# Kernel tuning notes

Hardware: AMD Instinct MI355X
Metric: run time of the kernel (lower is better)

Reference implementation:

```python
import jax, jax.numpy as jnp
import numpy as np

N = 50000      # nodes
E = 400000     # edges
IN_DIM = 128
HID = 64
HEADS1 = 4
OUT_DIM = 64
NEG_SLOPE = 0.2


def _gat_layer(x, W, attn_l, attn_r, bias, src, dst, heads, out_feats):
    # x: [N, F_in]; W: [F_in, heads*out]; attn_l/attn_r: [heads, out]; bias: [heads*out]
    n = x.shape[0]
    feat = (x @ W).reshape(n, heads, out_feats)              # [N, H, D]
    el = jnp.sum(feat * attn_l, axis=-1)                     # [N, H]
    er = jnp.sum(feat * attn_r, axis=-1)                     # [N, H]
    e = jax.nn.leaky_relu(el[src] + er[dst], NEG_SLOPE)      # [E, H]
    # segment softmax over incoming edges per destination node
    emax = jax.ops.segment_max(e, dst, num_segments=n)       # [N, H]
    ex = jnp.exp(e - emax[dst])                              # [E, H]
    denom = jax.ops.segment_sum(ex, dst, num_segments=n)     # [N, H]
    alpha = ex / denom[dst]                                  # [E, H]
    msg = alpha[:, :, None] * feat[src]                      # [E, H, D]
    rst = jax.ops.segment_sum(msg, dst, num_segments=n)      # [N, H, D]
    return rst + bias.reshape(1, heads, out_feats)


def setup_inputs() -> dict:
    key = jax.random.key(0)
    ks = jax.random.split(key, 12)
    features = jax.random.normal(ks[0], (N, IN_DIM), dtype=jnp.float32)
    src = jax.random.randint(ks[1], (E,), 0, N, dtype=jnp.int32)
    dst = jax.random.randint(ks[2], (E,), 0, N, dtype=jnp.int32)
    s1 = 1.0 / np.sqrt(IN_DIM)
    s2 = 1.0 / np.sqrt(HEADS1 * HID)
    W1 = jax.random.normal(ks[3], (IN_DIM, HEADS1 * HID), dtype=jnp.float32) * s1
    attn_l1 = jax.random.normal(ks[4], (HEADS1, HID), dtype=jnp.float32) * 0.1
    attn_r1 = jax.random.normal(ks[5], (HEADS1, HID), dtype=jnp.float32) * 0.1
    b1 = jnp.zeros((HEADS1 * HID,), dtype=jnp.float32)
    W2 = jax.random.normal(ks[6], (HEADS1 * HID, OUT_DIM), dtype=jnp.float32) * s2
    attn_l2 = jax.random.normal(ks[7], (1, OUT_DIM), dtype=jnp.float32) * 0.1
    attn_r2 = jax.random.normal(ks[8], (1, OUT_DIM), dtype=jnp.float32) * 0.1
    b2 = jnp.zeros((OUT_DIM,), dtype=jnp.float32)
    return {"features": features, "src": src, "dst": dst,
            "W1": W1, "attn_l1": attn_l1, "attn_r1": attn_r1, "b1": b1,
            "W2": W2, "attn_l2": attn_l2, "attn_r2": attn_r2, "b2": b2}


def reference(features, src, dst, W1, attn_l1, attn_r1, b1, W2, attn_l2, attn_r2, b2):
    h = _gat_layer(features, W1, attn_l1, attn_r1, b1, src, dst, HEADS1, HID)  # [N, 4, 64]
    h = h.reshape(h.shape[0], -1)                                             # flatten heads
    h = _gat_layer(h, W2, attn_l2, attn_r2, b2, src, dst, 1, OUT_DIM)         # [N, 1, 64]
    return h
```

## Files before the change

kernel.cpp:

```cpp
#include <hip/hip_runtime.h>
#include <hip/hip_bf16.h>

#define N_NODES 50000
#define N_EDGES 400000
#define IN_DIM 128
#define HID 64
#define HEADS 4
#define L1_OUT (HEADS * HID)
#define OUT_DIM 64
#define NEG_SLOPE 0.2f
#define SCAN_B 256
#define HIST_B 1563

typedef short bf16x8 __attribute__((ext_vector_type(8)));
typedef float f32x4 __attribute__((ext_vector_type(4)));

__device__ __forceinline__ float leaky(float x) { return x > 0.f ? x : NEG_SLOPE * x; }

__device__ __forceinline__ unsigned short bfh(float x) {
    unsigned u = __float_as_uint(x);
    return (unsigned short)((u + 0x7fffu + ((u >> 16) & 1u)) >> 16);
}
__device__ __forceinline__ float fb(unsigned short h) {
    return __uint_as_float(((unsigned)h) << 16);
}

__global__ void hist_wprep_kernel(const int* __restrict__ dst, int* __restrict__ cnt,
                                  const float* __restrict__ W1, const float* __restrict__ W2,
                                  unsigned short* __restrict__ W1fh, unsigned short* __restrict__ W1fl,
                                  unsigned short* __restrict__ W2fh, unsigned short* __restrict__ W2fl) {
    int bid = blockIdx.x;
    if (bid < HIST_B) {
        int e = bid * 256 + threadIdx.x;
        if (e < N_EDGES) atomicAdd(&cnt[dst[e]], 1);
        return;
    }
    int s = (bid - HIST_B) * 256 + threadIdx.x;
    if (s < 4096) {
        int lane = s & 63, ks = (s >> 6) & 3, ntile = s >> 8;
        int n = ntile * 16 + (lane & 15);
        int kb = ks * 32 + (lane >> 4) * 8;
#pragma unroll
        for (int j = 0; j < 8; ++j) {
            float w = W1[(kb + j) * L1_OUT + n];
            unsigned short h = bfh(w);
            W1fh[s * 8 + j] = h;
            W1fl[s * 8 + j] = bfh(w - fb(h));
        }
    } else if (s < 6144) {
        int s2 = s - 4096;
        int lane = s2 & 63, ks = (s2 >> 6) & 7, ntile = s2 >> 9;
        int n = ntile * 16 + (lane & 15);
        int kb = ks * 32 + (lane >> 4) * 8;
#pragma unroll
        for (int j = 0; j < 8; ++j) {
            float w = W2[(kb + j) * OUT_DIM + n];
            unsigned short h = bfh(w);
            W2fh[s2 * 8 + j] = h;
            W2fl[s2 * 8 + j] = bfh(w - fb(h));
        }
    }
}

__global__ void scanA_kernel(const int* __restrict__ cnt, int* __restrict__ texcl,
                             int* __restrict__ bsum) {
    __shared__ int sh[SCAN_B];
    int tid = threadIdx.x;
    int i = blockIdx.x * SCAN_B + tid;
    int v = (i < N_NODES) ? cnt[i] : 0;
    sh[tid] = v;
    __syncthreads();
    for (int off = 1; off < SCAN_B; off <<= 1) {
        int t = (tid >= off) ? sh[tid - off] : 0;
        __syncthreads();
        sh[tid] += t;
        __syncthreads();
    }
    if (i < N_NODES) texcl[i] = sh[tid] - v;
    if (tid == SCAN_B - 1) bsum[blockIdx.x] = sh[tid];
}

__global__ void scanB_kernel(const int* __restrict__ bsum, int* __restrict__ bexcl, int nb) {
    __shared__ int sh[SCAN_B];
    int tid = threadIdx.x;
    int v = (tid < nb) ? bsum[tid] : 0;
    sh[tid] = v;
    __syncthreads();
    for (int off = 1; off < SCAN_B; off <<= 1) {
        int t = (tid >= off) ? sh[tid - off] : 0;
        __syncthreads();
        sh[tid] += t;
        __syncthreads();
    }
    if (tid < nb) bexcl[tid] = sh[tid] - v;
}

__global__ void scanC_kernel(const int* __restrict__ texcl, const int* __restrict__ bexcl,
                             int* __restrict__ row) {
    int i = blockIdx.x * blockDim.x + threadIdx.x;
    if (i < N_NODES) row[i] = texcl[i] + bexcl[i >> 8];
    if (blockIdx.x == 0 && threadIdx.x == 0) row[N_NODES] = N_EDGES;
}

__global__ void fill_kernel(const int* __restrict__ src, const int* __restrict__ dst,
                            const int* __restrict__ row, int* __restrict__ fc,
                            int* __restrict__ perm_src) {
    int e = blockIdx.x * blockDim.x + threadIdx.x;
    if (e >= N_EDGES) return;
    int d = dst[e];
    int p = row[d] + atomicAdd(&fc[d], 1);
    perm_src[p] = src[e];
}

__global__ __launch_bounds__(512) void gemm1_kernel(const float* __restrict__ X,
                                                    const unsigned short* __restrict__ W1fh,
                                                    const unsigned short* __restrict__ W1fl,
                                                    const float* __restrict__ al1,
                                                    const float* __restrict__ ar1,
                                                    unsigned short* __restrict__ feat1b,
                                                    float* __restrict__ el1,
                                                    float* __restrict__ er1) {
    __shared__ unsigned short Ah[4 * 4 * 64 * 8];
    __shared__ unsigned short Al[4 * 4 * 64 * 8];
    int t = threadIdx.x;
    int m0 = blockIdx.x * 64;

    {
        int m = t >> 3;
        int k0 = (t & 7) * 16;
        int mfrag = m >> 4, mrow = m & 15;
        bool valid = (m0 + m) < N_NODES;
        const float4* xr = (const float4*)&X[(size_t)(m0 + m) * IN_DIM];
#pragma unroll
        for (int g = 0; g < 4; ++g) {
            int k = k0 + g * 4;
            float4 v = valid ? xr[k >> 2] : float4{0.f, 0.f, 0.f, 0.f};
            int kstep = k >> 5, kk = k & 31;
            int lane = mrow + 16 * (kk >> 3);
            int j0 = kk & 7;
            int base = ((mfrag * 4 + kstep) * 64 + lane) * 8 + j0;
            unsigned short h0 = bfh(v.x), h1 = bfh(v.y), h2 = bfh(v.z), h3 = bfh(v.w);
            *(ushort4*)&Ah[base] = make_ushort4(h0, h1, h2, h3);
            *(ushort4*)&Al[base] = make_ushort4(bfh(v.x - fb(h0)), bfh(v.y - fb(h1)),
                                                bfh(v.z - fb(h2)), bfh(v.w - fb(h3)));
        }
    }
    __syncthreads();

    int w = t >> 6, lane = t & 63;
    int wr = w >> 2, wc = w & 3;
    f32x4 acc[2][4];
#pragma unroll
    for (int mi = 0; mi < 2; ++mi)
#pragma unroll
        for (int nf = 0; nf < 4; ++nf) acc[mi][nf] = f32x4{0.f, 0.f, 0.f, 0.f};

#pragma unroll
    for (int kstep = 0; kstep < 4; ++kstep) {
        bf16x8 a_h[2], a_l[2];
#pragma unroll
        for (int mi = 0; mi < 2; ++mi) {
            int slot = (((wr * 2 + mi) * 4 + kstep) * 64 + lane) * 8;
            a_h[mi] = *(const bf16x8*)&Ah[slot];
            a_l[mi] = *(const bf16x8*)&Al[slot];
        }
#pragma unroll
        for (int nf = 0; nf < 4; ++nf) {
            int slot = (((wc * 4 + nf) * 4 + kstep) * 64 + lane) * 8;
            bf16x8 b_h = *(const bf16x8*)&W1fh[slot];
            bf16x8 b_l = *(const bf16x8*)&W1fl[slot];
#pragma unroll
            for (int mi = 0; mi < 2; ++mi) {
                acc[mi][nf] = __builtin_amdgcn_mfma_f32_16x16x32_bf16(a_h[mi], b_h, acc[mi][nf], 0, 0, 0);
                acc[mi][nf] = __builtin_amdgcn_mfma_f32_16x16x32_bf16(a_h[mi], b_l, acc[mi][nf], 0, 0, 0);
                acc[mi][nf] = __builtin_amdgcn_mfma_f32_16x16x32_bf16(a_l[mi], b_h, acc[mi][nf], 0, 0, 0);
            }
        }
    }

    int fq = lane >> 4, fr = lane & 15;
#pragma unroll
    for (int mi = 0; mi < 2; ++mi) {
#pragma unroll
        for (int j = 0; j < 4; ++j) {
            int r = m0 + wr * 32 + mi * 16 + fq * 4 + j;
            if (r >= N_NODES) continue;
#pragma unroll
            for (int nf = 0; nf < 4; ++nf) {
                int c = wc * 64 + nf * 16 + fr;
                feat1b[(size_t)r * L1_OUT + c] = bfh(acc[mi][nf][j]);
            }
        }
    }

    float al_v[4], ar_v[4];
#pragma unroll
    for (int nf = 0; nf < 4; ++nf) {
        al_v[nf] = al1[wc * 64 + nf * 16 + fr];
        ar_v[nf] = ar1[wc * 64 + nf * 16 + fr];
    }
#pragma unroll
    for (int mi = 0; mi < 2; ++mi) {
#pragma unroll
        for (int j = 0; j < 4; ++j) {
            float l = 0.f, r = 0.f;
#pragma unroll
            for (int nf = 0; nf < 4; ++nf) {
                l += acc[mi][nf][j] * al_v[nf];
                r += acc[mi][nf][j] * ar_v[nf];
            }
#pragma unroll
            for (int off = 1; off < 16; off <<= 1) {
                l += __shfl_xor(l, off, 64);
                r += __shfl_xor(r, off, 64);
            }
            int rr = m0 + wr * 32 + mi * 16 + fq * 4 + j;
            if (fr == 0 && rr < N_NODES) {
                el1[rr * HEADS + wc] = l;
                er1[rr * HEADS + wc] = r;
            }
        }
    }
}

__global__ __launch_bounds__(256) void layer2_kernel(const int* __restrict__ row,
                                                     const int* __restrict__ perm_src,
                                                     const float* __restrict__ el1,
                                                     const float* __restrict__ er1,
                                                     const unsigned short* __restrict__ feat1b,
                                                     const float* __restrict__ b1,
                                                     const unsigned short* __restrict__ W2fh,
                                                     const unsigned short* __restrict__ W2fl,
                                                     const float* __restrict__ al2,
                                                     const float* __restrict__ ar2,
                                                     unsigned short* __restrict__ feat2b,
                                                     float* __restrict__ el2,
                                                     float* __restrict__ er2) {
    __shared__ unsigned short Ah[2 * 8 * 64 * 8];
    __shared__ unsigned short Al[2 * 8 * 64 * 8];
    __shared__ float pl[2][2][16], pr[2][2][16];
    int t = threadIdx.x;
    int w = t >> 6, lane = t & 63;
    int n0 = blockIdx.x * 32;

    float4 b1v = *(const float4*)&b1[lane * 4];
    const ushort4* f4 = (const ushort4*)feat1b;

#pragma unroll 1
    for (int it = 0; it < 8; ++it) {
        int d = n0 + it * 4 + w;
        float4 acc = {0.f, 0.f, 0.f, 0.f};
        bool valid = d < N_NODES;
        if (valid) {
            int base = row[d], deg = row[d + 1] - base;
            if (deg > 0 && deg <= 16) {
                int h = lane >> 4, jj = lane & 15;
                int s_reg = (jj < deg) ? perm_src[base + jj] : 0;
                float er_d = er1[d * HEADS + h];
                float sc = (jj < deg) ? leaky(el1[s_reg * HEADS + h] + er_d) : -1e30f;
                float m = sc;
                m = fmaxf(m, __shfl_xor(m, 1, 64));
                m = fmaxf(m, __shfl_xor(m, 2, 64));
                m = fmaxf(m, __shfl_xor(m, 4, 64));
                m = fmaxf(m, __shfl_xor(m, 8, 64));
                float ex = (jj < deg) ? __expf(sc - m) : 0.f;
                float ss = ex;
                ss += __shfl_xor(ss, 1, 64);
                ss += __shfl_xor(ss, 2, 64);
                ss += __shfl_xor(ss, 4, 64);
                ss += __shfl_xor(ss, 8, 64);
                float alpha = ex / ss;
                int hb = lane & 48;
                float4 A0 = {0.f,0.f,0.f,0.f}, A1 = {0.f,0.f,0.f,0.f};
                float4 A2 = {0.f,0.f,0.f,0.f}, A3 = {0.f,0.f,0.f,0.f};
                int j = 0;
                for (; j + 3 < deg; j += 4) {
                    int s0 = __shfl(s_reg, j), s1 = __shfl(s_reg, j + 1);
                    int s2 = __shfl(s_reg, j + 2), s3 = __shfl(s_reg, j + 3);
                    float a0 = __shfl(alpha, hb + j), a1 = __shfl(alpha, hb + j + 1);
                    float a2 = __shfl(alpha, hb + j + 2), a3 = __shfl(alpha, hb + j + 3);
                    ushort4 f0 = f4[(size_t)s0 * 64 + lane];
                    ushort4 f1 = f4[(size_t)s1 * 64 + lane];
                    ushort4 f2 = f4[(size_t)s2 * 64 + lane];
                    ushort4 f3 = f4[(size_t)s3 * 64 + lane];
                    A0.x += a0 * fb(f0.x); A0.y += a0 * fb(f0.y); A0.z += a0 * fb(f0.z); A0.w += a0 * fb(f0.w);
                    A1.x += a1 * fb(f1.x); A1.y += a1 * fb(f1.y); A1.z += a1 * fb(f1.z); A1.w += a1 * fb(f1.w);
                    A2.x += a2 * fb(f2.x); A2.y += a2 * fb(f2.y); A2.z += a2 * fb(f2.z); A2.w += a2 * fb(f2.w);
                    A3.x += a3 * fb(f3.x); A3.y += a3 * fb(f3.y); A3.z += a3 * fb(f3.z); A3.w += a3 * fb(f3.w);
                }
                for (; j < deg; ++j) {
                    int s0 = __shfl(s_reg, j);
                    float a0 = __shfl(alpha, hb + j);
                    ushort4 f0 = f4[(size_t)s0 * 64 + lane];
                    A0.x += a0 * fb(f0.x); A0.y += a0 * fb(f0.y); A0.z += a0 * fb(f0.z); A0.w += a0 * fb(f0.w);
                }
                acc.x = A0.x + A1.x + A2.x + A3.x;
                acc.y = A0.y + A1.y + A2.y + A3.y;
                acc.z = A0.z + A1.z + A2.z + A3.z;
                acc.w = A0.w + A1.w + A2.w + A3.w;
            } else if (deg > 16) {
                float mh0, mh1, mh2, mh3, iv0, iv1, iv2, iv3;
#pragma unroll
                for (int h = 0; h < 4; ++h) {
                    float er_dh = er1[d * HEADS + h];
                    float m = -1e30f;
                    for (int j = lane; j < deg; j += 64)
                        m = fmaxf(m, leaky(el1[perm_src[base + j] * HEADS + h] + er_dh));
#pragma unroll
                    for (int off = 1; off < 64; off <<= 1) m = fmaxf(m, __shfl_xor(m, off, 64));
                    float ss = 0.f;
                    for (int j = lane; j < deg; j += 64)
                        ss += __expf(leaky(el1[perm_src[base + j] * HEADS + h] + er_dh) - m);
#pragma unroll
                    for (int off = 1; off < 64; off <<= 1) ss += __shfl_xor(ss, off, 64);
                    float iv = 1.f / ss;
                    if (h == 0) { mh0 = m; iv0 = iv; }
                    else if (h == 1) { mh1 = m; iv1 = iv; }
                    else if (h == 2) { mh2 = m; iv2 = iv; }
                    else { mh3 = m; iv3 = iv; }
                }
                int hh = lane >> 4;
                float m_s = hh == 0 ? mh0 : hh == 1 ? mh1 : hh == 2 ? mh2 : mh3;
                float iv_s = hh == 0 ? iv0 : hh == 1 ? iv1 : hh == 2 ? iv2 : iv3;
                float er_s = er1[d * HEADS + hh];
                for (int j = 0; j < deg; ++j) {
                    int s = perm_src[base + j];
                    float a = __expf(leaky(el1[s * HEADS + hh] + er_s) - m_s) * iv_s;
                    ushort4 f0 = f4[(size_t)s * 64 + lane];
                    acc.x += a * fb(f0.x); acc.y += a * fb(f0.y);
                    acc.z += a * fb(f0.z); acc.w += a * fb(f0.w);
                }
            }
            acc.x += b1v.x; acc.y += b1v.y; acc.z += b1v.z; acc.w += b1v.w;
        }
        int m = it * 4 + w;
        int mfrag = m >> 4, mrow = m & 15;
        int c = lane * 4;
        int kstep = c >> 5;
        int fraglane = mrow + 16 * ((c & 31) >> 3);
        int j0 = c & 7;
        int basei = ((mfrag * 8 + kstep) * 64 + fraglane) * 8 + j0;
        unsigned short h0 = bfh(acc.x), h1 = bfh(acc.y), h2 = bfh(acc.z), h3 = bfh(acc.w);
        *(ushort4*)&Ah[basei] = make_ushort4(h0, h1, h2, h3);
        *(ushort4*)&Al[basei] = make_ushort4(bfh(acc.x - fb(h0)), bfh(acc.y - fb(h1)),
                                             bfh(acc.z - fb(h2)), bfh(acc.w - fb(h3)));
    }
    __syncthreads();

    int mi = w >> 1, nh = w & 1;
    f32x4 acc2[2];
    acc2[0] = f32x4{0.f, 0.f, 0.f, 0.f};
    acc2[1] = f32x4{0.f, 0.f, 0.f, 0.f};

#pragma unroll
    for (int ks = 0; ks < 8; ++ks) {
        int aslot = ((mi * 8 + ks) * 64 + lane) * 8;
        bf16x8 a_h = *(const bf16x8*)&Ah[aslot];
        bf16x8 a_l = *(const bf16x8*)&Al[aslot];
#pragma unroll
        for (int nf = 0; nf < 2; ++nf) {
            int ntile = nh * 2 + nf;
            int slot = ((ntile * 8 + ks) * 64 + lane) * 8;
            bf16x8 b_h = *(const bf16x8*)&W2fh[slot];
            bf16x8 b_l = *(const bf16x8*)&W2fl[slot];
            acc2[nf] = __builtin_amdgcn_mfma_f32_16x16x32_bf16(a_h, b_h, acc2[nf], 0, 0, 0);
            acc2[nf] = __builtin_amdgcn_mfma_f32_16x16x32_bf16(a_h, b_l, acc2[nf], 0, 0, 0);
            acc2[nf] = __builtin_amdgcn_mfma_f32_16x16x32_bf16(a_l, b_h, acc2[nf], 0, 0, 0);
        }
    }

    int fq = lane >> 4, fr = lane & 15;
#pragma unroll
    for (int j = 0; j < 4; ++j) {
        int r = n0 + mi * 16 + fq * 4 + j;
        if (r >= N_NODES) continue;
#pragma unroll
        for (int nf = 0; nf < 2; ++nf) {
            int c = (nh * 2 + nf) * 16 + fr;
            feat2b[(size_t)r * OUT_DIM + c] = bfh(acc2[nf][j]);
        }
    }

    float al_v[2], ar_v[2];
#pragma unroll
    for (int nf = 0; nf < 2; ++nf) {
        al_v[nf] = al2[(nh * 2 + nf) * 16 + fr];
        ar_v[nf] = ar2[(nh * 2 + nf) * 16 + fr];
    }
#pragma unroll
    for (int j = 0; j < 4; ++j) {
        float l = acc2[0][j] * al_v[0] + acc2[1][j] * al_v[1];
        float r = acc2[0][j] * ar_v[0] + acc2[1][j] * ar_v[1];
#pragma unroll
        for (int off = 1; off < 16; off <<= 1) {
            l += __shfl_xor(l, off, 64);
            r += __shfl_xor(r, off, 64);
        }
        if (fr == 0) {
            pl[nh][mi][fq * 4 + j] = l;
            pr[nh][mi][fq * 4 + j] = r;
        }
    }
    __syncthreads();
    if (t < 32) {
        int n = n0 + t;
        if (n < N_NODES) {
            int mi2 = t >> 4, rr = t & 15;
            el2[n] = pl[0][mi2][rr] + pl[1][mi2][rr];
            er2[n] = pr[0][mi2][rr] + pr[1][mi2][rr];
        }
    }
}

__global__ __launch_bounds__(256) void gather2_kernel(const int* __restrict__ row,
                                                      const int* __restrict__ perm_src,
                                                      const float* __restrict__ el2,
                                                      const float* __restrict__ er2,
                                                      const unsigned short* __restrict__ feat2b,
                                                      const float* __restrict__ b2,
                                                      float* __restrict__ out) {
    int tid = threadIdx.x;
    int w = tid >> 6, lane = tid & 63;
    int d = blockIdx.x * 4 + w;
    int base = row[d], deg = row[d + 1] - base;
    float bias = b2[lane];
    if (deg == 0) {
        out[(size_t)d * OUT_DIM + lane] = bias;
        return;
    }
    if (deg <= 64) {
        int s_reg = (lane < deg) ? perm_src[base + lane] : 0;
        float er_d = er2[d];
        float sc = (lane < deg) ? leaky(el2[s_reg] + er_d) : -1e30f;
        float m = sc;
#pragma unroll
        for (int off = 1; off < 64; off <<= 1) m = fmaxf(m, __shfl_xor(m, off, 64));
        float ex = (lane < deg) ? __expf(sc - m) : 0.f;
        float ss = ex;
#pragma unroll
        for (int off = 1; off < 64; off <<= 1) ss += __shfl_xor(ss, off, 64);
        float alpha = ex / ss;
        float a0 = 0.f, a1 = 0.f, a2 = 0.f, a3 = 0.f;
        int j = 0;
        for (; j + 3 < deg; j += 4) {
            int s0 = __shfl(s_reg, j), s1 = __shfl(s_reg, j + 1);
            int s2 = __shfl(s_reg, j + 2), s3 = __shfl(s_reg, j + 3);
            float w0 = __shfl(alpha, j), w1 = __shfl(alpha, j + 1);
            float w2 = __shfl(alpha, j + 2), w3 = __shfl(alpha, j + 3);
            a0 += w0 * fb(feat2b[(size_t)s0 * OUT_DIM + lane]);
            a1 += w1 * fb(feat2b[(size_t)s1 * OUT_DIM + lane]);
            a2 += w2 * fb(feat2b[(size_t)s2 * OUT_DIM + lane]);
            a3 += w3 * fb(feat2b[(size_t)s3 * OUT_DIM + lane]);
        }
        for (; j < deg; ++j) {
            int s0 = __shfl(s_reg, j);
            float w0 = __shfl(alpha, j);
            a0 += w0 * fb(feat2b[(size_t)s0 * OUT_DIM + lane]);
        }
        out[(size_t)d * OUT_DIM + lane] = a0 + a1 + a2 + a3 + bias;
    } else {
        float er_d = er2[d];
        float m = -1e30f;
        for (int j = lane; j < deg; j += 64)
            m = fmaxf(m, leaky(el2[perm_src[base + j]] + er_d));
#pragma unroll
        for (int off = 1; off < 64; off <<= 1) m = fmaxf(m, __shfl_xor(m, off, 64));
        float ss = 0.f;
        for (int j = lane; j < deg; j += 64)
            ss += __expf(leaky(el2[perm_src[base + j]] + er_d) - m);
#pragma unroll
        for (int off = 1; off < 64; off <<= 1) ss += __shfl_xor(ss, off, 64);
        float inv = 1.f / ss;
        float a0 = 0.f;
        for (int j = 0; j < deg; ++j) {
            int s = perm_src[base + j];
            float a = __expf(leaky(el2[s] + er_d) - m) * inv;
            a0 += a * fb(feat2b[(size_t)s * OUT_DIM + lane]);
        }
        out[(size_t)d * OUT_DIM + lane] = a0 + bias;
    }
}

extern "C" void kernel_launch(void* const* d_in, const int* in_sizes, int n_in,
                              void* d_out, int out_size, void* d_ws, size_t ws_size,
                              hipStream_t stream) {
    const float* features = (const float*)d_in[0];
    const int* src = (const int*)d_in[1];
    const int* dst = (const int*)d_in[2];
    const float* W1 = (const float*)d_in[3];
    const float* al1 = (const float*)d_in[4];
    const float* ar1 = (const float*)d_in[5];
    const float* b1 = (const float*)d_in[6];
    const float* W2 = (const float*)d_in[7];
    const float* al2 = (const float*)d_in[8];
    const float* ar2 = (const float*)d_in[9];
    const float* b2 = (const float*)d_in[10];
    float* out = (float*)d_out;

    float* ws = (float*)d_ws;
    float* el1 = ws;
    float* er1 = el1 + N_NODES * HEADS;
    float* el2 = er1 + N_NODES * HEADS;
    float* er2 = el2 + N_NODES;
    unsigned short* feat1b = (unsigned short*)(er2 + N_NODES);
    unsigned short* feat2b = feat1b + (size_t)N_NODES * L1_OUT;
    unsigned short* W1fh = feat2b + (size_t)N_NODES * OUT_DIM;
    unsigned short* W1fl = W1fh + 32768;
    unsigned short* W2fh = W1fl + 32768;
    unsigned short* W2fl = W2fh + 16384;
    int* cnt = (int*)(W2fl + 16384);
    int* fc = cnt + N_NODES;
    int* texcl = fc + N_NODES;
    int* bsum = texcl + N_NODES;
    int* bexcl = bsum + 256;
    int* row = bexcl + 256;
    int* perm_src = row + N_NODES + 1;

    const int nscan = (N_NODES + SCAN_B - 1) / SCAN_B;

    hipMemsetAsync(cnt, 0, (size_t)2 * N_NODES * sizeof(int), stream);

    hist_wprep_kernel<<<HIST_B + 24, 256, 0, stream>>>(dst, cnt, W1, W2, W1fh, W1fl, W2fh, W2fl);
    scanA_kernel<<<nscan, SCAN_B, 0, stream>>>(cnt, texcl, bsum);
    scanB_kernel<<<1, SCAN_B, 0, stream>>>(bsum, bexcl, nscan);
    scanC_kernel<<<(N_NODES + 255) / 256, 256, 0, stream>>>(texcl, bexcl, row);
    fill_kernel<<<(N_EDGES + 255) / 256, 256, 0, stream>>>(src, dst, row, fc, perm_src);

    gemm1_kernel<<<(N_NODES + 63) / 64, 512, 0, stream>>>(features, W1fh, W1fl, al1, ar1,
                                                          feat1b, el1, er1);
    layer2_kernel<<<(N_NODES + 31) / 32, 256, 0, stream>>>(row, perm_src, el1, er1, feat1b,
                                                           b1, W2fh, W2fl, al2, ar2,
                                                           feat2b, el2, er2);
    gather2_kernel<<<N_NODES / 4, 256, 0, stream>>>(row, perm_src, el2, er2, feat2b, b2, out);
}
```

Baseline: 181.7 us.

## Use 512-thread blocks in layer2 with one MFMA tile per wave and swizzled LDS

Doubles the layer2 block size to 8 waves, so each wave aggregates 4 destination nodes instead of 8, and gives each wave a single 16x16 output tile in the small GEMM. An XOR swizzle is added to the LDS A-fragment layout to reduce bank conflicts on the stores and loads. The aim is more parallelism in the latency-bound gather phase and shorter per-wave serial work. The cost is a larger cross-wave reduction of the el2/er2 partials and higher register pressure under launch_bounds(512,8).

```diff
diff --git a/kernel.cpp b/kernel.cpp
--- a/kernel.cpp
+++ b/kernel.cpp
@@ -23,6 +23,10 @@
 }
 __device__ __forceinline__ float fb(unsigned short h) {
     return __uint_as_float(((unsigned)h) << 16);
+}
+
+__device__ __forceinline__ int swzA(int u) {
+    return u ^ (((u >> 6) & 7) ^ (((u >> 4) & 3) << 1));
 }
 
 __global__ void hist_wprep_kernel(const int* __restrict__ dst, int* __restrict__ cnt,
@@ -223,22 +227,22 @@
     }
 }
 
-__global__ __launch_bounds__(256) void layer2_kernel(const int* __restrict__ row,
-                                                     const int* __restrict__ perm_src,
-                                                     const float* __restrict__ el1,
-                                                     const float* __restrict__ er1,
-                                                     const unsigned short* __restrict__ feat1b,
-                                                     const float* __restrict__ b1,
-                                                     const unsigned short* __restrict__ W2fh,
-                                                     const unsigned short* __restrict__ W2fl,
-                                                     const float* __restrict__ al2,
-                                                     const float* __restrict__ ar2,
-                                                     unsigned short* __restrict__ feat2b,
-                                                     float* __restrict__ el2,
-                                                     float* __restrict__ er2) {
+__global__ __launch_bounds__(512, 8) void layer2_kernel(const int* __restrict__ row,
+                                                        const int* __restrict__ perm_src,
+                                                        const float* __restrict__ el1,
+                                                        const float* __restrict__ er1,
+                                                        const unsigned short* __restrict__ feat1b,
+                                                        const float* __restrict__ b1,
+                                                        const unsigned short* __restrict__ W2fh,
+                                                        const unsigned short* __restrict__ W2fl,
+                                                        const float* __restrict__ al2,
+                                                        const float* __restrict__ ar2,
+                                                        unsigned short* __restrict__ feat2b,
+                                                        float* __restrict__ el2,
+                                                        float* __restrict__ er2) {
     __shared__ unsigned short Ah[2 * 8 * 64 * 8];
     __shared__ unsigned short Al[2 * 8 * 64 * 8];
-    __shared__ float pl[2][2][16], pr[2][2][16];
+    __shared__ float pl[2][4][16], pr[2][4][16];
     int t = threadIdx.x;
     int w = t >> 6, lane = t & 63;
     int n0 = blockIdx.x * 32;
@@ -247,8 +251,8 @@
     const ushort4* f4 = (const ushort4*)feat1b;
 
 #pragma unroll 1
-    for (int it = 0; it < 8; ++it) {
-        int d = n0 + it * 4 + w;
+    for (int it = 0; it < 4; ++it) {
+        int d = n0 + it * 8 + w;
         float4 acc = {0.f, 0.f, 0.f, 0.f};
         bool valid = d < N_NODES;
         if (valid) {
@@ -333,13 +337,13 @@
             }
             acc.x += b1v.x; acc.y += b1v.y; acc.z += b1v.z; acc.w += b1v.w;
         }
-        int m = it * 4 + w;
+        int m = it * 8 + w;
         int mfrag = m >> 4, mrow = m & 15;
         int c = lane * 4;
         int kstep = c >> 5;
-        int fraglane = mrow + 16 * ((c & 31) >> 3);
-        int j0 = c & 7;
-        int basei = ((mfrag * 8 + kstep) * 64 + fraglane) * 8 + j0;
+        int g = (c & 31) >> 3;
+        int u = (mfrag * 8 + kstep) * 64 + mrow + 16 * g;
+        int basei = swzA(u) * 8 + (c & 7);
         unsigned short h0 = bfh(acc.x), h1 = bfh(acc.y), h2 = bfh(acc.z), h3 = bfh(acc.w);
         *(ushort4*)&Ah[basei] = make_ushort4(h0, h1, h2, h3);
         *(ushort4*)&Al[basei] = make_ushort4(bfh(acc.x - fb(h0)), bfh(acc.y - fb(h1)),
@@ -347,58 +351,46 @@
     }
     __syncthreads();
 
-    int mi = w >> 1, nh = w & 1;
-    f32x4 acc2[2];
-    acc2[0] = f32x4{0.f, 0.f, 0.f, 0.f};
-    acc2[1] = f32x4{0.f, 0.f, 0.f, 0.f};
+    int mi = w & 1, ntile = w >> 1;
+    f32x4 acc2 = f32x4{0.f, 0.f, 0.f, 0.f};
 
 #pragma unroll
     for (int ks = 0; ks < 8; ++ks) {
-        int aslot = ((mi * 8 + ks) * 64 + lane) * 8;
+        int aslot = swzA((mi * 8 + ks) * 64 + lane) * 8;
         bf16x8 a_h = *(const bf16x8*)&Ah[aslot];
         bf16x8 a_l = *(const bf16x8*)&Al[aslot];
-#pragma unroll
-        for (int nf = 0; nf < 2; ++nf) {
-            int ntile = nh * 2 + nf;
-            int slot = ((ntile * 8 + ks) * 64 + lane) * 8;
-            bf16x8 b_h = *(const bf16x8*)&W2fh[slot];
-            bf16x8 b_l = *(const bf16x8*)&W2fl[slot];
-            acc2[nf] = __builtin_amdgcn_mfma_f32_16x16x32_bf16(a_h, b_h, acc2[nf], 0, 0, 0);
-            acc2[nf] = __builtin_amdgcn_mfma_f32_16x16x32_bf16(a_h, b_l, acc2[nf], 0, 0, 0);
-            acc2[nf] = __builtin_amdgcn_mfma_f32_16x16x32_bf16(a_l, b_h, acc2[nf], 0, 0, 0);
-        }
+        int slot = ((ntile * 8 + ks) * 64 + lane) * 8;
+        bf16x8 b_h = *(const bf16x8*)&W2fh[slot];
+        bf16x8 b_l = *(const bf16x8*)&W2fl[slot];
+        acc2 = __builtin_amdgcn_mfma_f32_16x16x32_bf16(a_h, b_h, acc2, 0, 0, 0);
+        acc2 = __builtin_amdgcn_mfma_f32_16x16x32_bf16(a_h, b_l, acc2, 0, 0, 0);
+        acc2 = __builtin_amdgcn_mfma_f32_16x16x32_bf16(a_l, b_h, acc2, 0, 0, 0);
     }
 
     int fq = lane >> 4, fr = lane & 15;
 #pragma unroll
     for (int j = 0; j < 4; ++j) {
         int r = n0 + mi * 16 + fq * 4 + j;
-        if (r >= N_NODES) continue;
-#pragma unroll
-        for (int nf = 0; nf < 2; ++nf) {
-            int c = (nh * 2 + nf) * 16 + fr;
-            feat2b[(size_t)r * OUT_DIM + c] = bfh(acc2[nf][j]);
-        }
-    }
-
-    float al_v[2], ar_v[2];
-#pragma unroll
-    for (int nf = 0; nf < 2; ++nf) {
-        al_v[nf] = al2[(nh * 2 + nf) * 16 + fr];
-        ar_v[nf] = ar2[(nh * 2 + nf) * 16 + fr];
-    }
+        if (r < N_NODES) {
+            int c = ntile * 16 + fr;
+            feat2b[(size_t)r * OUT_DIM + c] = bfh(acc2[j]);
+        }
+    }
+
+    float al_v = al2[ntile * 16 + fr];
+    float ar_v = ar2[ntile * 16 + fr];
 #pragma unroll
     for (int j = 0; j < 4; ++j) {
-        float l = acc2[0][j] * al_v[0] + acc2[1][j] * al_v[1];
-        float r = acc2[0][j] * ar_v[0] + acc2[1][j] * ar_v[1];
+        float l = acc2[j] * al_v;
+        float r = acc2[j] * ar_v;
 #pragma unroll
         for (int off = 1; off < 16; off <<= 1) {
             l += __shfl_xor(l, off, 64);
             r += __shfl_xor(r, off, 64);
         }
         if (fr == 0) {
-            pl[nh][mi][fq * 4 + j] = l;
-            pr[nh][mi][fq * 4 + j] = r;
+            pl[mi][ntile][fq * 4 + j] = l;
+            pr[mi][ntile][fq * 4 + j] = r;
         }
     }
     __syncthreads();
@@ -406,8 +398,8 @@
         int n = n0 + t;
         if (n < N_NODES) {
             int mi2 = t >> 4, rr = t & 15;
-            el2[n] = pl[0][mi2][rr] + pl[1][mi2][rr];
-            er2[n] = pr[0][mi2][rr] + pr[1][mi2][rr];
+            el2[n] = pl[mi2][0][rr] + pl[mi2][1][rr] + pl[mi2][2][rr] + pl[mi2][3][rr];
+            er2[n] = pr[mi2][0][rr] + pr[mi2][1][rr] + pr[mi2][2][rr] + pr[mi2][3][rr];
         }
     }
 }
@@ -528,7 +520,7 @@
 
     gemm1_kernel<<<(N_NODES + 63) / 64, 512, 0, stream>>>(features, W1fh, W1fl, al1, ar1,
                                                           feat1b, el1, er1);
-    layer2_kernel<<<(N_NODES + 31) / 32, 256, 0, stream>>>(row, perm_src, el1, er1, feat1b,
+    layer2_kernel<<<(N_NODES + 31) / 32, 512, 0, stream>>>(row, perm_src, el1, er1, feat1b,
                                                            b1, W2fh, W2fl, al2, ar2,
                                                            feat2b, el2, er2);
     gather2_kernel<<<N_NODES / 4, 256, 0, stream>>>(row, perm_src, el2, er2, feat2b, b2, out);
```

Result: faster. 163.2 us (-10.2%).
